# Performance work log

Measured on AMD Instinct MI355X. Metric: run time of the kernel, lower is better.

Reference implementation:

```python
import jax, jax.numpy as jnp
import numpy as np

N = 16384      # nodes per NodeFlow layer
E = 262144     # edges per block (avg degree 16)
T = 327680     # total interpro indices (~20 per node)
P = 20000      # protein embedding table rows
INTERPRO = 30000
D_ESM = 1280
D = 1024
L = 5000       # labels_num
G = 2          # num_gcn


def setup_inputs() -> dict:
    key = jax.random.key(0)
    ks = jax.random.split(key, 16)
    protein_embedding = jax.random.normal(ks[0], (P, D_ESM), jnp.float32) * 0.02
    interpro_weight = jax.random.normal(ks[1], (INTERPRO, D), jnp.float32) * 0.02
    W_esm = jax.random.normal(ks[2], (D, D_ESM), jnp.float32) * (1.0 / np.sqrt(D_ESM))
    b_esm = jnp.zeros((D,), jnp.float32)
    bias1 = jnp.zeros((D,), jnp.float32)
    bias2 = jnp.zeros((D,), jnp.float32)
    w = jnp.ones((2,), jnp.float32)
    W_upd = jax.random.normal(ks[3], (G, D, 2 * D), jnp.float32) * (1.0 / np.sqrt(2 * D))
    b_upd = jnp.zeros((G, D), jnp.float32)
    W_out = jax.random.normal(ks[4], (L, D + D_ESM), jnp.float32) * (1.0 / np.sqrt(D + D_ESM))
    b_out = jnp.zeros((L,), jnp.float32)
    self_w = jax.random.uniform(ks[5], (E,), jnp.float32)
    ppi_w = jax.random.uniform(ks[6], (E,), jnp.float32)
    inputs = jax.random.randint(ks[7], (N,), 0, P)
    interpro_idx = jax.random.randint(ks[8], (T,), 0, INTERPRO)
    off = jnp.sort(jax.random.randint(ks[9], (N + 1,), 0, T))
    interpro_off = off.at[0].set(0).at[-1].set(T)  # include_last_offset convention
    src = jax.random.randint(ks[10], (E,), 0, N)
    dst = jax.random.randint(ks[11], (E,), 0, N)
    target_id = jax.random.randint(ks[12], (N,), 0, P)
    return dict(protein_embedding=protein_embedding, interpro_weight=interpro_weight,
                W_esm=W_esm, b_esm=b_esm, bias1=bias1, bias2=bias2, w=w,
                W_upd=W_upd, b_upd=b_upd, W_out=W_out, b_out=b_out,
                self_w=self_w, ppi_w=ppi_w, inputs=inputs,
                interpro_idx=interpro_idx, interpro_off=interpro_off,
                src=src, dst=dst, target_id=target_id)


def reference(protein_embedding, interpro_weight, W_esm, b_esm, bias1, bias2, w,
              W_upd, b_upd, W_out, b_out, self_w, ppi_w,
              inputs, interpro_idx, interpro_off, src, dst, target_id):
    # x1: ESM branch -> relu(Linear(esm[inputs]) + bias1)
    x1 = jax.nn.relu(protein_embedding[inputs] @ W_esm.T + b_esm + bias1)  # [N, D]
    # x2: EmbeddingBag(mode='sum', include_last_offset=True) + bias2
    seg = jnp.searchsorted(interpro_off, jnp.arange(T), side='right') - 1  # bag id per index
    bags = jax.ops.segment_sum(interpro_weight[interpro_idx], seg, num_segments=N)
    x2 = jax.nn.relu(bags + bias2)  # [N, D]
    # learned softmax mixture of the two branches
    sm = jax.nn.softmax(w)
    h = sm[0] * x1 + sm[1] * x2  # [N, D]
    # message passing layers: u_mul_e + sum for 'self' and 'ppi' edge weights,
    # then NodeUpdate: relu(Linear(cat(ppi_out, res))). Dropout is identity (eval).
    for i in range(G):
        msg = h[src]  # [E, D] irregular gather
        res = jax.ops.segment_sum(msg * self_w[:, None], dst, num_segments=N)
        ppi_out = jax.ops.segment_sum(msg * ppi_w[:, None], dst, num_segments=N)
        h = jax.nn.relu(jnp.concatenate([ppi_out, res], axis=1) @ W_upd[i].T + b_upd[i])
    last = jnp.concatenate([h, protein_embedding[target_id]], axis=1)  # [N, D+D_ESM]
    return last @ W_out.T + b_out  # [N, L]
```

## Files before the change

kernel.cpp:

```cpp
#include <hip/hip_runtime.h>

typedef unsigned short u16;
typedef u16 u16x4 __attribute__((ext_vector_type(4)));
typedef u16 u16x8 __attribute__((ext_vector_type(8)));
typedef float f32x4 __attribute__((ext_vector_type(4)));
typedef __bf16 bf16x8 __attribute__((ext_vector_type(8)));

#define NN 16384
#define EE 262144
#define DD 1024
#define DESM 1280
#define LL 5000

static __device__ __forceinline__ u16 f2bf(float f) {
  unsigned u = __float_as_uint(f);
  u += 0x7FFF + ((u >> 16) & 1);
  return (u16)(u >> 16);
}
static __device__ __forceinline__ float bf2f(u16 h) {
  return __uint_as_float(((unsigned)h) << 16);
}

__global__ void cast_rows_k(const float* __restrict__ src, int scols,
                            const int* __restrict__ rowidx,
                            u16* __restrict__ dst, int dld, int dcol0,
                            int rows, int cols8 ) {
  long total = (long)rows * cols8;
  for (long i = blockIdx.x * (long)blockDim.x + threadIdx.x; i < total;
       i += (long)gridDim.x * blockDim.x) {
    int r = (int)(i / cols8);
    int k8 = (int)(i % cols8);
    int sr = rowidx ? rowidx[r] : r;
    const f32x4* s = (const f32x4*)(src + (size_t)sr * scols + (size_t)k8 * 8);
    f32x4 a = s[0], b = s[1];
    u16x8 o;
    o[0] = f2bf(a[0]); o[1] = f2bf(a[1]); o[2] = f2bf(a[2]); o[3] = f2bf(a[3]);
    o[4] = f2bf(b[0]); o[5] = f2bf(b[1]); o[6] = f2bf(b[2]); o[7] = f2bf(b[3]);
    *(u16x8*)(dst + (size_t)r * dld + dcol0 + (size_t)k8 * 8) = o;
  }
}

__global__ void embed_bag_k(const float* __restrict__ W, const int* __restrict__ idx,
                            const int* __restrict__ off, const float* __restrict__ bias2,
                            float* __restrict__ x2pre) {
  int n = blockIdx.x;
  int t = threadIdx.x;
  int beg = off[n], end = off[n + 1];
  f32x4 acc = {0.f, 0.f, 0.f, 0.f};
  for (int p = beg; p < end; ++p) {
    int row = idx[p];
    f32x4 v = *(const f32x4*)(W + (size_t)row * DD + t * 4);
    acc += v;
  }
  acc += *(const f32x4*)(bias2 + t * 4);
  *(f32x4*)(x2pre + (size_t)n * DD + t * 4) = acc;
}

__global__ void hist_k(const int* __restrict__ dst, int* __restrict__ counts) {
  int e = blockIdx.x * blockDim.x + threadIdx.x;
  if (e < EE) atomicAdd(&counts[dst[e]], 1);
}

__global__ void scan_k(const int* __restrict__ counts, int* __restrict__ row_off) {
  __shared__ int sh[256];
  int t = threadIdx.x;
  int s = 0;
  for (int i = 0; i < 64; ++i) s += counts[t * 64 + i];
  sh[t] = s;
  __syncthreads();
  if (t == 0) {
    int run = 0;
    for (int i = 0; i < 256; ++i) { int v = sh[i]; sh[i] = run; run += v; }
    row_off[NN] = run;
  }
  __syncthreads();
  int run = sh[t];
  for (int i = 0; i < 64; ++i) { row_off[t * 64 + i] = run; run += counts[t * 64 + i]; }
}

__global__ void scatter_k(const int* __restrict__ dst, int* __restrict__ cursor,
                          int* __restrict__ perm) {
  int e = blockIdx.x * blockDim.x + threadIdx.x;
  if (e < EE) {
    int pos = atomicAdd(&cursor[dst[e]], 1);
    perm[pos] = e;
  }
}

__global__ void aggregate_k(const u16* __restrict__ h, const int* __restrict__ row_off,
                            const int* __restrict__ perm, const float* __restrict__ self_w,
                            const float* __restrict__ ppi_w, const int* __restrict__ src,
                            u16* __restrict__ cat) {
  int n = blockIdx.x;
  int t = threadIdx.x;
  int beg = row_off[n], end = row_off[n + 1];
  f32x4 res = {0.f, 0.f, 0.f, 0.f}, ppi = {0.f, 0.f, 0.f, 0.f};
  for (int p = beg; p < end; ++p) {
    int e = perm[p];
    int s = src[e];
    float ws = self_w[e], wp = ppi_w[e];
    u16x4 m = *(const u16x4*)(h + (size_t)s * DD + t * 4);
    f32x4 mf = {bf2f(m[0]), bf2f(m[1]), bf2f(m[2]), bf2f(m[3])};
    res += ws * mf;
    ppi += wp * mf;
  }
  u16x4 o0, o1;
  o0[0] = f2bf(ppi[0]); o0[1] = f2bf(ppi[1]); o0[2] = f2bf(ppi[2]); o0[3] = f2bf(ppi[3]);
  o1[0] = f2bf(res[0]); o1[1] = f2bf(res[1]); o1[2] = f2bf(res[2]); o1[3] = f2bf(res[3]);
  *(u16x4*)(cat + (size_t)n * 2048 + t * 4) = o0;
  *(u16x4*)(cat + (size_t)n * 2048 + DD + t * 4) = o1;
}

static __device__ __forceinline__ void stage_half(const char* Gb, size_t ldb, int rowbase,
                                                  int rowmax, int kbyte, char* lds_half_w,
                                                  int s_rowoff, int s_inner) {
#pragma unroll
  for (int j = 0; j < 2; ++j) {
    int row = rowbase + j * 128 + s_rowoff;
    if (row > rowmax) row = rowmax;
    const char* src = Gb + (size_t)row * ldb + kbyte + s_inner;
    __builtin_amdgcn_global_load_lds(
        (const __attribute__((address_space(1))) void*)src,
        (__attribute__((address_space(3))) void*)(lds_half_w + j * 8192), 16, 0, 0);
  }
}

static __device__ __forceinline__ bf16x8 ldr(const char* kh, int row, int slot) {
  unsigned a = (unsigned)row * 64u +
               ((((unsigned)slot << 4) ^ ((((unsigned)row >> 1) & 3u) << 4)));
  return *(const bf16x8*)(kh + a);
}

template <int MODE>
__global__ __launch_bounds__(512, 2) void gemm8_k(
    const u16* __restrict__ A, const u16* __restrict__ B, int M, int N, int K,
    void* __restrict__ Cout, int ldc, const float* __restrict__ bias0,
    const float* __restrict__ bias1, const float* __restrict__ x2pre,
    const float* __restrict__ wmix) {
  __shared__ char lds[131072];
  char* ldsA = lds;
  char* ldsB = lds + 65536;
  const int tid = threadIdx.x;
  const int lane = tid & 63;
  const int wid = tid >> 6;
  const int wr = wid >> 2;
  const int wc = wid & 3;
  const int nwg = gridDim.x * gridDim.y;
  const int flat = blockIdx.x + gridDim.x * blockIdx.y;
  const int swz = (flat & 7) * (nwg >> 3) + (flat >> 3);
  const int row0 = (swz / gridDim.x) * 256;
  const int col0 = (swz % gridDim.x) * 256;
  const int NT = K >> 6;
  const size_t lda = (size_t)K * 2;
  const char* Ab = (const char*)A;
  const char* Bb = (const char*)B;
  const int l15 = lane & 15;
  const int slot = lane >> 4;
  const int s_rowoff = wid * 16 + (lane >> 2);
  const int s_inner = (((lane & 3) << 4) ^ (((lane >> 3) & 3) << 4));
  const int wb = wid * 1024;

  f32x4 acc[8][4];
#pragma unroll
  for (int m = 0; m < 8; ++m)
#pragma unroll
    for (int n = 0; n < 4; ++n) acc[m][n] = (f32x4){0.f, 0.f, 0.f, 0.f};

  stage_half(Bb, lda, col0, N - 1, 0,   ldsB + 0 + wb, s_rowoff, s_inner);
  stage_half(Ab, lda, row0, M - 1, 0,   ldsA + 0 + wb, s_rowoff, s_inner);
  stage_half(Bb, lda, col0, N - 1, 64,  ldsB + 16384 + wb, s_rowoff, s_inner);
  stage_half(Ab, lda, row0, M - 1, 64,  ldsA + 16384 + wb, s_rowoff, s_inner);
  if (NT > 1) {
    stage_half(Bb, lda, col0, N - 1, 128, ldsB + 32768 + wb, s_rowoff, s_inner);
    stage_half(Ab, lda, row0, M - 1, 128, ldsA + 32768 + wb, s_rowoff, s_inner);
    stage_half(Bb, lda, col0, N - 1, 192, ldsB + 49152 + wb, s_rowoff, s_inner);
  } else {
    stage_half(Bb, lda, col0, N - 1, 0,  ldsB + 32768 + wb, s_rowoff, s_inner);
    stage_half(Ab, lda, row0, M - 1, 0,  ldsA + 32768 + wb, s_rowoff, s_inner);
    stage_half(Bb, lda, col0, N - 1, 0,  ldsB + 49152 + wb, s_rowoff, s_inner);
  }
  asm volatile("s_waitcnt vmcnt(6)" ::: "memory");
  __builtin_amdgcn_s_barrier();

  for (int t = 0; t < NT; ++t) {
    const int d = t & 1;
    char* Ad = ldsA + d * 32768;
    char* Bd = ldsB + d * 32768;
    const char* Akh0 = Ad;
    const char* Akh1 = Ad + 16384;
    const char* Bkh0 = Bd;
    const char* Bkh1 = Bd + 16384;
    const int ts1 = (t + 1 < NT) ? t + 1 : NT - 1;
    const int ts2 = (t + 2 < NT) ? t + 2 : NT - 1;
    bf16x8 af[4], bq[4];

#pragma unroll
    for (int m = 0; m < 4; ++m) af[m] = ldr(Akh0, wr * 128 + m * 16 + l15, slot);
#pragma unroll
    for (int n = 0; n < 4; ++n) bq[n] = ldr(Bkh0, wc * 64 + n * 16 + l15, slot);
    stage_half(Ab, lda, row0, M - 1, ts1 * 128 + 64,
               ldsA + ((t + 1) & 1) * 32768 + 16384 + wb, s_rowoff, s_inner);
    __builtin_amdgcn_s_barrier();
    asm volatile("s_waitcnt lgkmcnt(0)" ::: "memory");
    __builtin_amdgcn_s_setprio(1);
#pragma unroll
    for (int m = 0; m < 4; ++m)
#pragma unroll
      for (int n = 0; n < 4; ++n)
        acc[m][n] = __builtin_amdgcn_mfma_f32_16x16x32_bf16(af[m], bq[n], acc[m][n], 0, 0, 0);
    __builtin_amdgcn_s_setprio(0);
    __builtin_amdgcn_s_barrier();

#pragma unroll
    for (int m = 0; m < 4; ++m) af[m] = ldr(Akh0, wr * 128 + (m + 4) * 16 + l15, slot);
    stage_half(Bb, lda, col0, N - 1, ts2 * 128, Bd + wb, s_rowoff, s_inner);
    __builtin_amdgcn_s_barrier();
    asm volatile("s_waitcnt lgkmcnt(0)" ::: "memory");
    __builtin_amdgcn_s_setprio(1);
#pragma unroll
    for (int m = 0; m < 4; ++m)
#pragma unroll
      for (int n = 0; n < 4; ++n)
        acc[m + 4][n] = __builtin_amdgcn_mfma_f32_16x16x32_bf16(af[m], bq[n], acc[m + 4][n], 0, 0, 0);
    __builtin_amdgcn_s_setprio(0);
    __builtin_amdgcn_s_barrier();

#pragma unroll
    for (int m = 0; m < 4; ++m) af[m] = ldr(Akh1, wr * 128 + (m + 4) * 16 + l15, slot);
#pragma unroll
    for (int n = 0; n < 4; ++n) bq[n] = ldr(Bkh1, wc * 64 + n * 16 + l15, slot);
    stage_half(Ab, lda, row0, M - 1, ts2 * 128, Ad + wb, s_rowoff, s_inner);
    __builtin_amdgcn_s_barrier();
    asm volatile("s_waitcnt lgkmcnt(0)" ::: "memory");
    __builtin_amdgcn_s_setprio(1);
#pragma unroll
    for (int m = 0; m < 4; ++m)
#pragma unroll
      for (int n = 0; n < 4; ++n)
        acc[m + 4][n] = __builtin_amdgcn_mfma_f32_16x16x32_bf16(af[m], bq[n], acc[m + 4][n], 0, 0, 0);
    __builtin_amdgcn_s_setprio(0);
    __builtin_amdgcn_s_barrier();

#pragma unroll
    for (int m = 0; m < 4; ++m) af[m] = ldr(Akh1, wr * 128 + m * 16 + l15, slot);
    stage_half(Bb, lda, col0, N - 1, ts2 * 128 + 64, Bd + 16384 + wb, s_rowoff, s_inner);
    __builtin_amdgcn_s_barrier();
    asm volatile("s_waitcnt lgkmcnt(0)" ::: "memory");
    __builtin_amdgcn_s_setprio(1);
#pragma unroll
    for (int m = 0; m < 4; ++m)
#pragma unroll
      for (int n = 0; n < 4; ++n)
        acc[m][n] = __builtin_amdgcn_mfma_f32_16x16x32_bf16(af[m], bq[n], acc[m][n], 0, 0, 0);
    __builtin_amdgcn_s_setprio(0);
    asm volatile("s_waitcnt vmcnt(6)" ::: "memory");
    __builtin_amdgcn_s_barrier();
  }

  float sm0 = 0.f, sm1 = 0.f;
  if (MODE == 0) {
    float w0 = wmix[0], w1 = wmix[1];
    float mx = fmaxf(w0, w1);
    float e0 = expf(w0 - mx), e1 = expf(w1 - mx);
    float inv = 1.f / (e0 + e1);
    sm0 = e0 * inv;
    sm1 = e1 * inv;
  }
  float bc[4];
  int cs[4];
#pragma unroll
  for (int n = 0; n < 4; ++n) {
    int c = col0 + wc * 64 + n * 16 + l15;
    cs[n] = c;
    bc[n] = (MODE == 2 && c >= N) ? 0.f : (bias0[c] + (MODE == 0 ? bias1[c] : 0.f));
  }
#pragma unroll
  for (int m = 0; m < 8; ++m) {
#pragma unroll
    for (int n = 0; n < 4; ++n) {
      int c = cs[n];
      if (MODE == 2 && c >= N) continue;
      int r0 = row0 + wr * 128 + m * 16 + slot * 4;
#pragma unroll
      for (int r = 0; r < 4; ++r) {
        float v = acc[m][n][r] + bc[n];
        int rr = r0 + r;
        if (MODE == 0) {
          float x1v = fmaxf(v, 0.f);
          float x2v = fmaxf(x2pre[(size_t)rr * DD + c], 0.f);
          ((u16*)Cout)[(size_t)rr * ldc + c] = f2bf(sm0 * x1v + sm1 * x2v);
        } else if (MODE == 1) {
          ((u16*)Cout)[(size_t)rr * ldc + c] = f2bf(fmaxf(v, 0.f));
        } else {
          ((float*)Cout)[(size_t)rr * ldc + c] = v;
        }
      }
    }
  }
}

extern "C" void kernel_launch(void* const* d_in, const int* in_sizes, int n_in,
                              void* d_out, int out_size, void* d_ws, size_t ws_size,
                              hipStream_t stream) {
  const float* esm   = (const float*)d_in[0];
  const float* ipw   = (const float*)d_in[1];
  const float* Wesm  = (const float*)d_in[2];
  const float* besm  = (const float*)d_in[3];
  const float* bias1 = (const float*)d_in[4];
  const float* bias2 = (const float*)d_in[5];
  const float* wmix  = (const float*)d_in[6];
  const float* Wupd  = (const float*)d_in[7];
  const float* bupd  = (const float*)d_in[8];
  const float* Wout  = (const float*)d_in[9];
  const float* bout  = (const float*)d_in[10];
  const float* selfw = (const float*)d_in[11];
  const float* ppiw  = (const float*)d_in[12];
  const int* inputs  = (const int*)d_in[13];
  const int* ipidx   = (const int*)d_in[14];
  const int* ipoff   = (const int*)d_in[15];
  const int* src     = (const int*)d_in[16];
  const int* dst     = (const int*)d_in[17];
  const int* tgt     = (const int*)d_in[18];
  float* out = (float*)d_out;

  char* ws = (char*)d_ws;
  size_t o = 0;
  auto take = [&](size_t b) {
    char* r = ws + o;
    o += (b + 255) & ~(size_t)255;
    return r;
  };
  u16* Wesm_b = (u16*)take(1024ull * 1280 * 2);
  u16* Wupd_b = (u16*)take(2ull * 1024 * 2048 * 2);
  u16* Wout_b = (u16*)take(5000ull * 2304 * 2);
  int* counts  = (int*)take((size_t)NN * 4);
  int* row_off = (int*)take((size_t)(NN + 1) * 4);
  int* cursor  = (int*)take((size_t)NN * 4);
  int* perm    = (int*)take((size_t)EE * 4);
  u16* h_b     = (u16*)take((size_t)NN * DD * 2);
  char* shared0 = ws + o;
  u16* A1    = (u16*)shared0;
  float* x2pre = (float*)(shared0 + (((size_t)NN * DESM * 2 + 255) & ~(size_t)255));
  u16* cat_b = (u16*)shared0;
  u16* A_last = (u16*)(shared0 + (((size_t)NN * 2048 * 2 + 255) & ~(size_t)255));

  cast_rows_k<<<2048, 256, 0, stream>>>(Wesm, 1280, nullptr, Wesm_b, 1280, 0, 1024, 160);
  cast_rows_k<<<2048, 256, 0, stream>>>(Wupd, 2048, nullptr, Wupd_b, 2048, 0, 2048, 256);
  cast_rows_k<<<2048, 256, 0, stream>>>(Wout, 2304, nullptr, Wout_b, 2304, 0, 5000, 288);

  embed_bag_k<<<NN, 256, 0, stream>>>(ipw, ipidx, ipoff, bias2, x2pre);

  cast_rows_k<<<4096, 256, 0, stream>>>(esm, 1280, inputs, A1, 1280, 0, NN, 160);

  hipMemsetAsync(counts, 0, (size_t)NN * 4, stream);
  hist_k<<<EE / 256, 256, 0, stream>>>(dst, counts);
  scan_k<<<1, 256, 0, stream>>>(counts, row_off);
  hipMemcpyAsync(cursor, row_off, (size_t)NN * 4, hipMemcpyDeviceToDevice, stream);
  scatter_k<<<EE / 256, 256, 0, stream>>>(dst, cursor, perm);

  gemm8_k<0><<<dim3(4, 64), 512, 0, stream>>>(A1, Wesm_b, NN, 1024, 1280, h_b, 1024,
                                              besm, bias1, x2pre, wmix);

  cast_rows_k<<<4096, 256, 0, stream>>>(esm, 1280, tgt, A_last, 2304, 1024, NN, 160);

  aggregate_k<<<NN, 256, 0, stream>>>(h_b, row_off, perm, selfw, ppiw, src, cat_b);
  gemm8_k<1><<<dim3(4, 64), 512, 0, stream>>>(cat_b, Wupd_b, NN, 1024, 2048, h_b, 1024,
                                              bupd, nullptr, nullptr, nullptr);

  aggregate_k<<<NN, 256, 0, stream>>>(h_b, row_off, perm, selfw, ppiw, src, cat_b);
  gemm8_k<1><<<dim3(4, 64), 512, 0, stream>>>(cat_b, Wupd_b + (size_t)1024 * 2048, NN, 1024,
                                              2048, A_last, 2304, bupd + 1024, nullptr,
                                              nullptr, nullptr);

  gemm8_k<2><<<dim3(20, 64), 512, 0, stream>>>(A_last, Wout_b, NN, 5000, 2304, out, 5000,
                                               bout, nullptr, nullptr, nullptr);
}
```

Measured before the change: 1.092 ms.

## Software-pipeline LDS fragment loads in GEMM and gather embedding bags from bf16 table

The GEMM main loop is restructured so the A fragments for the next phase load while the current phase's MFMAs run, using ping-pong register sets (afP/afQ). The per-phase lgkmcnt(0) waits are removed, sched_barrier is added, and the prologue staging order and vmcnt thresholds change. Separately, the interpro embedding table is cast to bf16 once so embedding-bag gathers read half the bytes, at the cost of an extra cast pass over the 30000x1024 table and bf16 rounding of the summed inputs. Workspace buffers are re-laid out so the bf16 table fits.

```diff
diff --git a/kernel.cpp b/kernel.cpp
--- a/kernel.cpp
+++ b/kernel.cpp
@@ -11,6 +11,7 @@
 #define DD 1024
 #define DESM 1280
 #define LL 5000
+#define IPN 30000
 
 static __device__ __forceinline__ u16 f2bf(float f) {
   unsigned u = __float_as_uint(f);
@@ -40,7 +41,7 @@
   }
 }
 
-__global__ void embed_bag_k(const float* __restrict__ W, const int* __restrict__ idx,
+__global__ void embed_bag_k(const u16* __restrict__ W, const int* __restrict__ idx,
                             const int* __restrict__ off, const float* __restrict__ bias2,
                             float* __restrict__ x2pre) {
   int n = blockIdx.x;
@@ -49,8 +50,9 @@
   f32x4 acc = {0.f, 0.f, 0.f, 0.f};
   for (int p = beg; p < end; ++p) {
     int row = idx[p];
-    f32x4 v = *(const f32x4*)(W + (size_t)row * DD + t * 4);
-    acc += v;
+    u16x4 v = *(const u16x4*)(W + (size_t)row * DD + t * 4);
+    acc[0] += bf2f(v[0]); acc[1] += bf2f(v[1]);
+    acc[2] += bf2f(v[2]); acc[3] += bf2f(v[3]);
   }
   acc += *(const f32x4*)(bias2 + t * 4);
   *(f32x4*)(x2pre + (size_t)n * DD + t * 4) = acc;
@@ -166,94 +168,89 @@
 #pragma unroll
     for (int n = 0; n < 4; ++n) acc[m][n] = (f32x4){0.f, 0.f, 0.f, 0.f};
 
-  stage_half(Bb, lda, col0, N - 1, 0,   ldsB + 0 + wb, s_rowoff, s_inner);
-  stage_half(Ab, lda, row0, M - 1, 0,   ldsA + 0 + wb, s_rowoff, s_inner);
-  stage_half(Bb, lda, col0, N - 1, 64,  ldsB + 16384 + wb, s_rowoff, s_inner);
-  stage_half(Ab, lda, row0, M - 1, 64,  ldsA + 16384 + wb, s_rowoff, s_inner);
-  if (NT > 1) {
-    stage_half(Bb, lda, col0, N - 1, 128, ldsB + 32768 + wb, s_rowoff, s_inner);
-    stage_half(Ab, lda, row0, M - 1, 128, ldsA + 32768 + wb, s_rowoff, s_inner);
-    stage_half(Bb, lda, col0, N - 1, 192, ldsB + 49152 + wb, s_rowoff, s_inner);
-  } else {
-    stage_half(Bb, lda, col0, N - 1, 0,  ldsB + 32768 + wb, s_rowoff, s_inner);
-    stage_half(Ab, lda, row0, M - 1, 0,  ldsA + 32768 + wb, s_rowoff, s_inner);
-    stage_half(Bb, lda, col0, N - 1, 0,  ldsB + 49152 + wb, s_rowoff, s_inner);
-  }
-  asm volatile("s_waitcnt vmcnt(6)" ::: "memory");
+  const int k1 = (NT > 1) ? 128 : 0;
+  stage_half(Bb, lda, col0, N - 1, 0,       ldsB + 0     + wb, s_rowoff, s_inner);
+  stage_half(Ab, lda, row0, M - 1, 0,       ldsA + 0     + wb, s_rowoff, s_inner);
+  stage_half(Ab, lda, row0, M - 1, 64,      ldsA + 16384 + wb, s_rowoff, s_inner);
+  stage_half(Bb, lda, col0, N - 1, 64,      ldsB + 16384 + wb, s_rowoff, s_inner);
+  stage_half(Bb, lda, col0, N - 1, k1,      ldsB + 32768 + wb, s_rowoff, s_inner);
+  stage_half(Ab, lda, row0, M - 1, k1,      ldsA + 32768 + wb, s_rowoff, s_inner);
+  stage_half(Bb, lda, col0, N - 1, k1 + 64, ldsB + 49152 + wb, s_rowoff, s_inner);
+  asm volatile("s_waitcnt vmcnt(10)" ::: "memory");
   __builtin_amdgcn_s_barrier();
+
+  bf16x8 afP[4], afQ[4], bq[4];
+#pragma unroll
+  for (int m = 0; m < 4; ++m) afP[m] = ldr(ldsA, wr * 128 + m * 16 + l15, slot);
 
   for (int t = 0; t < NT; ++t) {
     const int d = t & 1;
     char* Ad = ldsA + d * 32768;
     char* Bd = ldsB + d * 32768;
-    const char* Akh0 = Ad;
     const char* Akh1 = Ad + 16384;
     const char* Bkh0 = Bd;
     const char* Bkh1 = Bd + 16384;
+    const char* AkhN0 = ldsA + (d ^ 1) * 32768;
     const int ts1 = (t + 1 < NT) ? t + 1 : NT - 1;
     const int ts2 = (t + 2 < NT) ? t + 2 : NT - 1;
-    bf16x8 af[4], bq[4];
-
-#pragma unroll
-    for (int m = 0; m < 4; ++m) af[m] = ldr(Akh0, wr * 128 + m * 16 + l15, slot);
+
 #pragma unroll
     for (int n = 0; n < 4; ++n) bq[n] = ldr(Bkh0, wc * 64 + n * 16 + l15, slot);
+#pragma unroll
+    for (int m = 0; m < 4; ++m) afQ[m] = ldr(Ad, wr * 128 + (m + 4) * 16 + l15, slot);
     stage_half(Ab, lda, row0, M - 1, ts1 * 128 + 64,
                ldsA + ((t + 1) & 1) * 32768 + 16384 + wb, s_rowoff, s_inner);
+    __builtin_amdgcn_sched_barrier(0);
+    __builtin_amdgcn_s_setprio(1);
+#pragma unroll
+    for (int m = 0; m < 4; ++m)
+#pragma unroll
+      for (int n = 0; n < 4; ++n)
+        acc[m][n] = __builtin_amdgcn_mfma_f32_16x16x32_bf16(afP[m], bq[n], acc[m][n], 0, 0, 0);
+    __builtin_amdgcn_s_setprio(0);
+    asm volatile("s_waitcnt vmcnt(8)" ::: "memory");
     __builtin_amdgcn_s_barrier();
-    asm volatile("s_waitcnt lgkmcnt(0)" ::: "memory");
+
+#pragma unroll
+    for (int m = 0; m < 4; ++m) afP[m] = ldr(Akh1, wr * 128 + (m + 4) * 16 + l15, slot);
+    stage_half(Bb, lda, col0, N - 1, ts2 * 128, Bd + wb, s_rowoff, s_inner);
+    __builtin_amdgcn_sched_barrier(0);
     __builtin_amdgcn_s_setprio(1);
 #pragma unroll
     for (int m = 0; m < 4; ++m)
 #pragma unroll
       for (int n = 0; n < 4; ++n)
-        acc[m][n] = __builtin_amdgcn_mfma_f32_16x16x32_bf16(af[m], bq[n], acc[m][n], 0, 0, 0);
+        acc[m + 4][n] = __builtin_amdgcn_mfma_f32_16x16x32_bf16(afQ[m], bq[n], acc[m + 4][n], 0, 0, 0);
     __builtin_amdgcn_s_setprio(0);
     __builtin_amdgcn_s_barrier();
 
 #pragma unroll
-    for (int m = 0; m < 4; ++m) af[m] = ldr(Akh0, wr * 128 + (m + 4) * 16 + l15, slot);
-    stage_half(Bb, lda, col0, N - 1, ts2 * 128, Bd + wb, s_rowoff, s_inner);
+    for (int n = 0; n < 4; ++n) bq[n] = ldr(Bkh1, wc * 64 + n * 16 + l15, slot);
+#pragma unroll
+    for (int m = 0; m < 4; ++m) afQ[m] = ldr(Akh1, wr * 128 + m * 16 + l15, slot);
+    stage_half(Ab, lda, row0, M - 1, ts2 * 128, Ad + wb, s_rowoff, s_inner);
+    __builtin_amdgcn_sched_barrier(0);
+    __builtin_amdgcn_s_setprio(1);
+#pragma unroll
+    for (int m = 0; m < 4; ++m)
+#pragma unroll
+      for (int n = 0; n < 4; ++n)
+        acc[m + 4][n] = __builtin_amdgcn_mfma_f32_16x16x32_bf16(afP[m], bq[n], acc[m + 4][n], 0, 0, 0);
+    __builtin_amdgcn_s_setprio(0);
+    asm volatile("s_waitcnt vmcnt(8)" ::: "memory");
     __builtin_amdgcn_s_barrier();
-    asm volatile("s_waitcnt lgkmcnt(0)" ::: "memory");
+
+#pragma unroll
+    for (int m = 0; m < 4; ++m) afP[m] = ldr(AkhN0, wr * 128 + m * 16 + l15, slot);
+    stage_half(Bb, lda, col0, N - 1, ts2 * 128 + 64, Bd + 16384 + wb, s_rowoff, s_inner);
+    __builtin_amdgcn_sched_barrier(0);
     __builtin_amdgcn_s_setprio(1);
 #pragma unroll
     for (int m = 0; m < 4; ++m)
 #pragma unroll
       for (int n = 0; n < 4; ++n)
-        acc[m + 4][n] = __builtin_amdgcn_mfma_f32_16x16x32_bf16(af[m], bq[n], acc[m + 4][n], 0, 0, 0);
+        acc[m][n] = __builtin_amdgcn_mfma_f32_16x16x32_bf16(afQ[m], bq[n], acc[m][n], 0, 0, 0);
     __builtin_amdgcn_s_setprio(0);
-    __builtin_amdgcn_s_barrier();
-
-#pragma unroll
-    for (int m = 0; m < 4; ++m) af[m] = ldr(Akh1, wr * 128 + (m + 4) * 16 + l15, slot);
-#pragma unroll
-    for (int n = 0; n < 4; ++n) bq[n] = ldr(Bkh1, wc * 64 + n * 16 + l15, slot);
-    stage_half(Ab, lda, row0, M - 1, ts2 * 128, Ad + wb, s_rowoff, s_inner);
-    __builtin_amdgcn_s_barrier();
-    asm volatile("s_waitcnt lgkmcnt(0)" ::: "memory");
-    __builtin_amdgcn_s_setprio(1);
-#pragma unroll
-    for (int m = 0; m < 4; ++m)
-#pragma unroll
-      for (int n = 0; n < 4; ++n)
-        acc[m + 4][n] = __builtin_amdgcn_mfma_f32_16x16x32_bf16(af[m], bq[n], acc[m + 4][n], 0, 0, 0);
-    __builtin_amdgcn_s_setprio(0);
-    __builtin_amdgcn_s_barrier();
-
-#pragma unroll
-    for (int m = 0; m < 4; ++m) af[m] = ldr(Akh1, wr * 128 + m * 16 + l15, slot);
-    stage_half(Bb, lda, col0, N - 1, ts2 * 128 + 64, Bd + 16384 + wb, s_rowoff, s_inner);
-    __builtin_amdgcn_s_barrier();
-    asm volatile("s_waitcnt lgkmcnt(0)" ::: "memory");
-    __builtin_amdgcn_s_setprio(1);
-#pragma unroll
-    for (int m = 0; m < 4; ++m)
-#pragma unroll
-      for (int n = 0; n < 4; ++n)
-        acc[m][n] = __builtin_amdgcn_mfma_f32_16x16x32_bf16(af[m], bq[n], acc[m][n], 0, 0, 0);
-    __builtin_amdgcn_s_setprio(0);
-    asm volatile("s_waitcnt vmcnt(6)" ::: "memory");
     __builtin_amdgcn_s_barrier();
   }
 
@@ -339,16 +336,20 @@
   int* perm    = (int*)take((size_t)EE * 4);
   u16* h_b     = (u16*)take((size_t)NN * DD * 2);
   char* shared0 = ws + o;
-  u16* A1    = (u16*)shared0;
-  float* x2pre = (float*)(shared0 + (((size_t)NN * DESM * 2 + 255) & ~(size_t)255));
-  u16* cat_b = (u16*)shared0;
-  u16* A_last = (u16*)(shared0 + (((size_t)NN * 2048 * 2 + 255) & ~(size_t)255));
+  size_t x2_b = ((size_t)NN * DD * 4 + 255) & ~(size_t)255;
+  size_t a1_b = ((size_t)NN * DESM * 2 + 255) & ~(size_t)255;
+  float* x2pre = (float*)shared0;
+  u16* A1     = (u16*)(shared0 + x2_b);
+  u16* ipw_b  = (u16*)(shared0 + x2_b + a1_b);
+  u16* cat_b  = (u16*)shared0;
+  u16* A_last = (u16*)(shared0 + x2_b);
 
   cast_rows_k<<<2048, 256, 0, stream>>>(Wesm, 1280, nullptr, Wesm_b, 1280, 0, 1024, 160);
   cast_rows_k<<<2048, 256, 0, stream>>>(Wupd, 2048, nullptr, Wupd_b, 2048, 0, 2048, 256);
   cast_rows_k<<<2048, 256, 0, stream>>>(Wout, 2304, nullptr, Wout_b, 2304, 0, 5000, 288);
-
-  embed_bag_k<<<NN, 256, 0, stream>>>(ipw, ipidx, ipoff, bias2, x2pre);
+  cast_rows_k<<<4096, 256, 0, stream>>>(ipw, 1024, nullptr, ipw_b, 1024, 0, IPN, 128);
+
+  embed_bag_k<<<NN, 256, 0, stream>>>(ipw_b, ipidx, ipoff, bias2, x2pre);
 
   cast_rows_k<<<4096, 256, 0, stream>>>(esm, 1280, inputs, A1, 1280, 0, NN, 160);
 
```

Result: faster. 1.021 ms (-6.5%).
